# Kernel tuning notes

Measured on AMD Instinct MI355X. Metric: run time of the kernel, lower is better.

## Reference

```python
import jax, jax.numpy as jnp
import numpy as np

N = 2048      # nodes (= in_features = out_features, forced by h0 @ adj)
C = 512       # channels
B = 8         # batch
NNZ = 65536   # number of edges (avg degree 32)
NEG = -9e15   # masked-fill value from the source


def setup_inputs() -> dict:
    key = jax.random.key(0)
    k1, k2, k3, k4 = jax.random.split(key, 4)
    x = jax.random.normal(k1, (B, C, N), dtype=jnp.float32)
    # xavier_normal_ with gain=0.01: std = gain * sqrt(2/(fan_in+fan_out))
    std = 0.01 * float(np.sqrt(2.0 / (N + N)))
    W1 = jax.random.normal(k2, (N, N), dtype=jnp.float32) * std
    W2 = jax.random.normal(k3, (N, N), dtype=jnp.float32) * std
    # e is initialized to 1 in the source; perturb so softmax is non-trivial
    e = 1.0 + 0.1 * jax.random.normal(k4, (NNZ,), dtype=jnp.float32)
    # flat row-major indices of mask nonzeros, unique + sorted (matches adj[mask] = e)
    rng = np.random.default_rng(0)
    edge_idx = np.sort(rng.choice(N * N, size=NNZ, replace=False)).astype(np.int64)
    return {"x": x, "W1": W1, "W2": W2, "e": e, "edge_idx": jnp.asarray(edge_idx)}


def reference(x, W1, W2, e, edge_idx):
    # h0, h1: [B, C, N]
    h0 = jnp.matmul(x, W1)
    h1 = jnp.matmul(x, W2)
    # scatter per-edge logits into dense [N, N], masked positions = -9e15
    logits = jnp.full((N * N,), NEG, dtype=jnp.float32).at[edge_idx].set(e)
    A = jax.nn.softmax(logits.reshape(N, N), axis=1)  # row-wise softmax
    diag = jnp.diagonal(A)                 # A * I  (self term, diagonal scaling)
    A_off = A - jnp.diag(diag)             # A * (1 - I)  (neighbor term)
    # h0 @ (A*I) == h0 scaled per-node by diag; h1 @ (A*(1-I)) dense GEMM
    out = h0 * diag[None, None, :] + jnp.matmul(h1, A_off)
    return out  # [B, C, N]; torch squeeze is a no-op here; bias=False
```

## Files before the change

kernel.cpp:

```cpp
#include <hip/hip_runtime.h>
#include <hip/hip_bf16.h>
#include <stdint.h>

#define NN 2048
#define LOG2NN 11
#define GK 2048
#define GNC 2048

typedef __bf16 bf16x8 __attribute__((ext_vector_type(8)));
typedef float f32x4 __attribute__((ext_vector_type(4)));

__device__ __forceinline__ ushort f2bf(float f) {
  uint32_t x = __float_as_uint(f);
  uint32_t r = (x + 0x7fffu + ((x >> 16) & 1u)) >> 16;
  return (ushort)r;
}

__device__ __forceinline__ int lower_bound32(const int* __restrict__ a, int n, int v) {
  int lo = 0, hi = n;
  while (lo < hi) {
    int mid = (lo + hi) >> 1;
    if (a[mid] < v) lo = mid + 1; else hi = mid;
  }
  return lo;
}

__global__ __launch_bounds__(256) void prep_kernel(
    const float* __restrict__ W1, const float* __restrict__ W2,
    ushort* __restrict__ WT, ushort* __restrict__ W2T,
    int* __restrict__ hist, int* __restrict__ ecnt,
    const int* __restrict__ idx, const float* __restrict__ e, int nnz,
    float* __restrict__ vals, float* __restrict__ diag, int* __restrict__ empty) {
  __shared__ float tile[64][65];
  const int bid = blockIdx.x;
  const int t = threadIdx.x;
  if (bid < 2048) {
    const int m = bid >> 10;
    const int rem = bid & 1023;
    const int r0 = (rem >> 5) * 64, c0 = (rem & 31) * 64;
    const float* in = m ? W2 : W1;
    ushort* out = m ? W2T : WT;
    const int tx = t & 15, ty = t >> 4;
#pragma unroll
    for (int i = 0; i < 4; ++i) {
      int r = i * 16 + ty;
      float4 v = *reinterpret_cast<const float4*>(&in[(size_t)(r0 + r) * NN + c0 + tx * 4]);
      tile[r][tx * 4 + 0] = v.x;
      tile[r][tx * 4 + 1] = v.y;
      tile[r][tx * 4 + 2] = v.z;
      tile[r][tx * 4 + 3] = v.w;
    }
    __syncthreads();
#pragma unroll
    for (int i = 0; i < 4; ++i) {
      int oc = i * 16 + ty;
      ushort4 o;
      o.x = f2bf(tile[tx * 4 + 0][oc]);
      o.y = f2bf(tile[tx * 4 + 1][oc]);
      o.z = f2bf(tile[tx * 4 + 2][oc]);
      o.w = f2bf(tile[tx * 4 + 3][oc]);
      *reinterpret_cast<ushort4*>(&out[(size_t)(c0 + oc) * NN + r0 + tx * 4]) = o;
    }
  } else {
    const int w = t >> 6, lane = t & 63;
    const int r = (bid - 2048) * 4 + w;
    int lo = lower_bound32(idx, nnz, r << LOG2NN);
    int hi = lower_bound32(idx, nnz, (r + 1) << LOG2NN);
    if (hi <= lo) {
      if (lane == 0) { diag[r] = 1.0f / NN; empty[r] = 1; atomicAdd(ecnt, 1); }
      return;
    }
    float m = -3.0e38f;
    for (int j = lo + lane; j < hi; j += 64) m = fmaxf(m, e[j]);
#pragma unroll
    for (int s = 32; s >= 1; s >>= 1) m = fmaxf(m, __shfl_xor(m, s));
    float sum = 0.f;
    for (int j = lo + lane; j < hi; j += 64) sum += expf(e[j] - m);
#pragma unroll
    for (int s = 32; s >= 1; s >>= 1) sum += __shfl_xor(sum, s);
    float inv = 1.0f / sum;
    float dv = 0.f;
    for (int j = lo + lane; j < hi; j += 64) {
      float v = expf(e[j] - m) * inv;
      vals[j] = v;
      int c = idx[j] & (NN - 1);
      if (c == r) dv = v;
      else atomicAdd(&hist[c], 1);
    }
#pragma unroll
    for (int s = 32; s >= 1; s >>= 1) dv += __shfl_xor(dv, s);
    if (lane == 0) { diag[r] = dv; empty[r] = 0; }
  }
}

__global__ __launch_bounds__(256) void scan_uw_kernel(
    const int* __restrict__ hist, int* __restrict__ base, int* __restrict__ cursor,
    const float* __restrict__ W2, const int* __restrict__ empty,
    const int* __restrict__ ecnt, float* __restrict__ uW) {
  if (blockIdx.x == 0) {
    const int l = threadIdx.x;
    if (l >= 64) return;
    int vals[32], pre[32];
    int run = 0;
#pragma unroll
    for (int j = 0; j < 32; ++j) {
      vals[j] = hist[l * 32 + j];
      pre[j] = run;
      run += vals[j];
    }
    int tot = run, inc = run;
#pragma unroll
    for (int s = 1; s < 64; s <<= 1) {
      int o = __shfl_up(inc, s);
      if (l >= s) inc += o;
    }
    int excl = inc - tot;
#pragma unroll
    for (int j = 0; j < 32; ++j) {
      int b = excl + pre[j];
      base[l * 32 + j] = b;
      cursor[l * 32 + j] = b;
    }
  } else {
    if (*ecnt == 0) return;
    int p = (blockIdx.x - 1) * 256 + threadIdx.x;
    float s = 0.f;
    for (int k = 0; k < NN; ++k)
      if (empty[k]) s += W2[(size_t)p * NN + k];
    uW[p] = s * (1.0f / NN);
  }
}

__global__ void scatter_kernel(const int* __restrict__ idx, const float* __restrict__ vals,
                               int nnz, int* __restrict__ cursor,
                               int* __restrict__ ek, float* __restrict__ ev) {
  int j = blockIdx.x * blockDim.x + threadIdx.x;
  if (j >= nnz) return;
  int f = idx[j];
  int c = f & (NN - 1), r = f >> LOG2NN;
  if (c != r) {
    int p = atomicAdd(&cursor[c], 1);
    ek[p] = r;
    ev[p] = vals[j];
  }
}

__global__ __launch_bounds__(256) void spmm_kernel(
    const int* __restrict__ ek, const float* __restrict__ ev,
    const int* __restrict__ base, const int* __restrict__ hist,
    const ushort* __restrict__ W2T,
    const float* __restrict__ diag, const int* __restrict__ empty,
    const float* __restrict__ uW, ushort* WT,
    const float* __restrict__ x, ushort* __restrict__ xb) {
  if (blockIdx.x >= 1024) {
    int i = ((int)blockIdx.x - 1024) * 256 + threadIdx.x;
    const float4* in4 = reinterpret_cast<const float4*>(x);
    float4 a = in4[2 * i];
    float4 b = in4[2 * i + 1];
    uint4 o;
    o.x = (uint32_t)f2bf(a.x) | ((uint32_t)f2bf(a.y) << 16);
    o.y = (uint32_t)f2bf(a.z) | ((uint32_t)f2bf(a.w) << 16);
    o.z = (uint32_t)f2bf(b.x) | ((uint32_t)f2bf(b.y) << 16);
    o.w = (uint32_t)f2bf(b.z) | ((uint32_t)f2bf(b.w) << 16);
    reinterpret_cast<uint4*>(xb)[i] = o;
    return;
  }
  const int w = threadIdx.x >> 6, lane = threadIdx.x & 63;
  const int n = blockIdx.x * 2 + (w >> 1);
  const int c0 = (w & 1) * 1024 + lane * 16;
  const int start = base[n], cnt = hist[n];
  float acc[2][8];
#pragma unroll
  for (int g = 0; g < 2; ++g) {
    float4 u0 = *reinterpret_cast<const float4*>(&uW[c0 + g * 8]);
    float4 u1 = *reinterpret_cast<const float4*>(&uW[c0 + g * 8 + 4]);
    acc[g][0] = u0.x; acc[g][1] = u0.y; acc[g][2] = u0.z; acc[g][3] = u0.w;
    acc[g][4] = u1.x; acc[g][5] = u1.y; acc[g][6] = u1.z; acc[g][7] = u1.w;
  }
  float d = diag[n];
  if (d != 0.f) {
#pragma unroll
    for (int g = 0; g < 2; ++g) {
      bf16x8 wd = *reinterpret_cast<const bf16x8*>(&WT[(size_t)n * NN + c0 + g * 8]);
#pragma unroll
      for (int j = 0; j < 8; ++j) acc[g][j] += d * (float)wd[j];
    }
  }
  int i = 0;
  for (; i + 4 <= cnt; i += 4) {
    int k[4];
    float v[4];
    bf16x8 wv[4][2];
#pragma unroll
    for (int e2 = 0; e2 < 4; ++e2) {
      k[e2] = ek[start + i + e2];
      v[e2] = ev[start + i + e2];
    }
#pragma unroll
    for (int e2 = 0; e2 < 4; ++e2)
#pragma unroll
      for (int g = 0; g < 2; ++g)
        wv[e2][g] = *reinterpret_cast<const bf16x8*>(&W2T[(size_t)k[e2] * NN + c0 + g * 8]);
#pragma unroll
    for (int e2 = 0; e2 < 4; ++e2)
#pragma unroll
      for (int g = 0; g < 2; ++g)
#pragma unroll
        for (int j = 0; j < 8; ++j)
          acc[g][j] += v[e2] * (float)wv[e2][g][j];
  }
  for (; i < cnt; ++i) {
    int k0 = ek[start + i];
    float v0 = ev[start + i];
#pragma unroll
    for (int g = 0; g < 2; ++g) {
      bf16x8 w0 = *reinterpret_cast<const bf16x8*>(&W2T[(size_t)k0 * NN + c0 + g * 8]);
#pragma unroll
      for (int j = 0; j < 8; ++j) acc[g][j] += v0 * (float)w0[j];
    }
  }
  if (empty[n]) {
#pragma unroll
    for (int g = 0; g < 2; ++g) {
      bf16x8 we = *reinterpret_cast<const bf16x8*>(&W2T[(size_t)n * NN + c0 + g * 8]);
#pragma unroll
      for (int j = 0; j < 8; ++j) acc[g][j] -= (1.0f / NN) * (float)we[j];
    }
  }
#pragma unroll
  for (int g = 0; g < 2; ++g) {
    uint4 o;
    o.x = (uint32_t)f2bf(acc[g][0]) | ((uint32_t)f2bf(acc[g][1]) << 16);
    o.y = (uint32_t)f2bf(acc[g][2]) | ((uint32_t)f2bf(acc[g][3]) << 16);
    o.z = (uint32_t)f2bf(acc[g][4]) | ((uint32_t)f2bf(acc[g][5]) << 16);
    o.w = (uint32_t)f2bf(acc[g][6]) | ((uint32_t)f2bf(acc[g][7]) << 16);
    *reinterpret_cast<uint4*>(&WT[(size_t)n * NN + c0 + g * 8]) = o;
  }
}

__device__ __forceinline__ void gload_lds16(const ushort* g, char* l) {
  __builtin_amdgcn_global_load_lds(
      (__attribute__((address_space(1))) uint32_t*)(uintptr_t)g,
      (__attribute__((address_space(3))) uint32_t*)l, 16, 0, 0);
}

#define NT 32

__global__ __launch_bounds__(512, 2)
void gemm8_kernel(const ushort* __restrict__ A, const ushort* __restrict__ Bt,
                  float* __restrict__ Cf) {
  __shared__ __align__(16) char smem[98304];
  const int t = threadIdx.x;
  const int wid = t >> 6, lane = t & 63;
  const int wm = wid >> 1, wn = wid & 1;
  const int fr = lane & 15, fg = lane >> 4;

  const int swz = ((int)blockIdx.x & 7) * 32 + ((int)blockIdx.x >> 3);
  const int m0 = (swz >> 4) * 256;
  const int n0 = (swz & 15) * 128;

  const int l8 = lane >> 3;
  const int scol = ((lane & 7) ^ l8) << 3;
  const int srow = wid * 8 + l8;

#define STGA(H, TAU) do {                                                      \
    const int _b = (TAU) & 1;                                                  \
    gload_lds16(A + (size_t)(m0 + (H) * 128 + srow) * GK + (TAU) * 64 + scol,  \
                smem + _b * 32768 + (H) * 16384 + wid * 1024);                 \
    gload_lds16(A + (size_t)(m0 + (H) * 128 + 64 + srow) * GK + (TAU) * 64 + scol, \
                smem + _b * 32768 + (H) * 16384 + 8192 + wid * 1024);          \
  } while (0)

#define STGB(TAU) do {                                                         \
    const int _b = (TAU) & 1;                                                  \
    gload_lds16(Bt + (size_t)(n0 + srow) * GK + (TAU) * 64 + scol,             \
                smem + 65536 + _b * 16384 + wid * 1024);                       \
    gload_lds16(Bt + (size_t)(n0 + 64 + srow) * GK + (TAU) * 64 + scol,        \
                smem + 65536 + _b * 16384 + 8192 + wid * 1024);                \
  } while (0)

  const int sw = (fr & 7) << 4;
  const int ko0 = (fg * 16) ^ sw;
  const int ko1 = (64 + fg * 16) ^ sw;

  f32x4 acc[4][4] = {};

  STGA(0, 0); STGA(1, 0); STGB(0);
  STGA(0, 1); STGA(1, 1); STGB(1);
  asm volatile("s_waitcnt vmcnt(6)" ::: "memory");
  __builtin_amdgcn_s_barrier();
  asm volatile("" ::: "memory");

  for (int kt = 0; kt < NT; ++kt) {
    const int b = kt & 1;
    const int t2 = (kt + 2) & (NT - 1);
    const char* Ab = smem + b * 32768;
    const char* Bb = smem + 65536 + b * 16384;
    bf16x8 aF[4][2], bF[4][2];
#pragma unroll
    for (int mf = 0; mf < 4; ++mf) {
      const int row = wm * 64 + mf * 16 + fr;
      const char* p = Ab + (row >> 7) * 16384 + (row & 127) * 128;
      aF[mf][0] = *reinterpret_cast<const bf16x8*>(p + ko0);
    }
#pragma unroll
    for (int nf = 0; nf < 4; ++nf) {
      const char* p = Bb + (wn * 64 + nf * 16 + fr) * 128;
      bF[nf][0] = *reinterpret_cast<const bf16x8*>(p + ko0);
    }
#pragma unroll
    for (int mf = 0; mf < 4; ++mf) {
      const int row = wm * 64 + mf * 16 + fr;
      const char* p = Ab + (row >> 7) * 16384 + (row & 127) * 128;
      aF[mf][1] = *reinterpret_cast<const bf16x8*>(p + ko1);
    }
#pragma unroll
    for (int nf = 0; nf < 4; ++nf) {
      const char* p = Bb + (wn * 64 + nf * 16 + fr) * 128;
      bF[nf][1] = *reinterpret_cast<const bf16x8*>(p + ko1);
    }
    __builtin_amdgcn_s_setprio(1);
#pragma unroll
    for (int mf = 0; mf < 4; ++mf)
#pragma unroll
      for (int nf = 0; nf < 4; ++nf)
        acc[mf][nf] = __builtin_amdgcn_mfma_f32_16x16x32_bf16(
            aF[mf][0], bF[nf][0], acc[mf][nf], 0, 0, 0);
#pragma unroll
    for (int mf = 0; mf < 4; ++mf)
#pragma unroll
      for (int nf = 0; nf < 4; ++nf)
        acc[mf][nf] = __builtin_amdgcn_mfma_f32_16x16x32_bf16(
            aF[mf][1], bF[nf][1], acc[mf][nf], 0, 0, 0);
    __builtin_amdgcn_s_setprio(0);
    __builtin_amdgcn_s_barrier();
    asm volatile("" ::: "memory");
    STGA(0, t2); STGA(1, t2); STGB(t2);
    asm volatile("s_waitcnt vmcnt(6)" ::: "memory");
    __builtin_amdgcn_s_barrier();
    asm volatile("" ::: "memory");
  }

  asm volatile("s_waitcnt vmcnt(0)" ::: "memory");
  const int cr = lane >> 4, cc = lane & 15;
#pragma unroll
  for (int mf = 0; mf < 4; ++mf)
#pragma unroll
    for (int nf = 0; nf < 4; ++nf)
#pragma unroll
      for (int q = 0; q < 4; ++q) {
        int gm = m0 + wm * 64 + mf * 16 + cr * 4 + q;
        int gn = n0 + wn * 64 + nf * 16 + cc;
        Cf[(size_t)gm * GNC + gn] = acc[mf][nf][q];
      }
}

extern "C" void kernel_launch(void* const* d_in, const int* in_sizes, int n_in,
                              void* d_out, int out_size, void* d_ws, size_t ws_size,
                              hipStream_t stream) {
  const float* x   = (const float*)d_in[0];
  const float* W1  = (const float*)d_in[1];
  const float* W2  = (const float*)d_in[2];
  const float* e   = (const float*)d_in[3];
  const int*   eix = (const int*)d_in[4];
  const int nnz = in_sizes[3];
  float* out = (float*)d_out;

  char* w = (char*)d_ws;
  ushort* W2T  = (ushort*)w; w += (size_t)NN * NN * 2;
  ushort* WT   = (ushort*)w; w += (size_t)NN * NN * 2;
  ushort* xb   = (ushort*)w; w += (size_t)4096 * NN * 2;
  float*  vals = (float*)w;  w += (size_t)nnz * 4;
  int*    ek   = (int*)w;    w += (size_t)nnz * 4;
  float*  ev   = (float*)w;  w += (size_t)nnz * 4;
  int*    base = (int*)w;    w += NN * 4;
  int*    curs = (int*)w;    w += NN * 4;
  float*  diag = (float*)w;  w += NN * 4;
  int*    empt = (int*)w;    w += NN * 4;
  int*    hist = (int*)w;    w += NN * 4;
  float*  uW   = (float*)w;  w += NN * 4;
  int*    ecnt = (int*)w;    w += 256;

  hipMemsetAsync(hist, 0, NN * 4 + NN * 4 + 256, stream);

  prep_kernel<<<dim3(2560), dim3(256), 0, stream>>>(W1, W2, WT, W2T,
                                                    hist, ecnt,
                                                    eix, e, nnz, vals, diag, empt);
  scan_uw_kernel<<<dim3(9), dim3(256), 0, stream>>>(hist, base, curs, W2, empt,
                                                    ecnt, uW);
  scatter_kernel<<<dim3((nnz + 255) / 256), dim3(256), 0, stream>>>(eix, vals, nnz,
                                                                    curs, ek, ev);
  spmm_kernel<<<dim3(5120), dim3(256), 0, stream>>>(ek, ev, base, hist, W2T,
                                                    diag, empt, uW, WT, x, xb);
  gemm8_kernel<<<dim3(256), dim3(512), 0, stream>>>(xb, WT, out);
}
```

Measured before the change: 111.2 us.

## Split GEMM k-tile into two half-stages with finer-grained async prefetch

Reorganizes the shared-memory layout of the bf16 GEMM so each 64-wide k-tile is stored as two 32-wide halves, and issues global-to-LDS loads per half so they interleave with the MFMA work on the other half. The XOR swizzle is removed in favour of a plain 64-byte row stride, and fragment register usage is halved. The aim is to overlap memory transfer with compute more finely. In exchange it adds an extra barrier per half-step, and the unswizzled layout may cause LDS bank conflicts.

```diff
diff --git a/kernel.cpp b/kernel.cpp
--- a/kernel.cpp
+++ b/kernel.cpp
@@ -259,84 +259,83 @@
   const int m0 = (swz >> 4) * 256;
   const int n0 = (swz & 15) * 128;
 
-  const int l8 = lane >> 3;
-  const int scol = ((lane & 7) ^ l8) << 3;
-  const int srow = wid * 8 + l8;
-
-#define STGA(H, TAU) do {                                                      \
-    const int _b = (TAU) & 1;                                                  \
-    gload_lds16(A + (size_t)(m0 + (H) * 128 + srow) * GK + (TAU) * 64 + scol,  \
-                smem + _b * 32768 + (H) * 16384 + wid * 1024);                 \
-    gload_lds16(A + (size_t)(m0 + (H) * 128 + 64 + srow) * GK + (TAU) * 64 + scol, \
-                smem + _b * 32768 + (H) * 16384 + 8192 + wid * 1024);          \
-  } while (0)
-
-#define STGB(TAU) do {                                                         \
-    const int _b = (TAU) & 1;                                                  \
-    gload_lds16(Bt + (size_t)(n0 + srow) * GK + (TAU) * 64 + scol,             \
-                smem + 65536 + _b * 16384 + wid * 1024);                       \
-    gload_lds16(Bt + (size_t)(n0 + 64 + srow) * GK + (TAU) * 64 + scol,        \
-                smem + 65536 + _b * 16384 + 8192 + wid * 1024);                \
-  } while (0)
-
-  const int sw = (fr & 7) << 4;
-  const int ko0 = (fg * 16) ^ sw;
-  const int ko1 = (64 + fg * 16) ^ sw;
+  const int crow = wid * 16 + (lane >> 2);
+  const int ccol = (lane & 3) * 8;
+
+#define STGA(H, KS, TAU)                                                       \
+  gload_lds16(A + (size_t)(m0 + (H) * 128 + crow) * GK + (TAU) * 64 + (KS) * 32 + ccol, \
+              smem + ((TAU) & 1) * 32768 + (KS) * 16384 + (H) * 8192 + wid * 1024)
+#define STGB(KS, TAU)                                                          \
+  gload_lds16(Bt + (size_t)(n0 + crow) * GK + (TAU) * 64 + (KS) * 32 + ccol,   \
+              smem + 65536 + ((TAU) & 1) * 16384 + (KS) * 8192 + wid * 1024)
 
   f32x4 acc[4][4] = {};
 
-  STGA(0, 0); STGA(1, 0); STGB(0);
-  STGA(0, 1); STGA(1, 1); STGB(1);
+  STGA(0, 0, 0); STGA(1, 0, 0); STGB(0, 0);
+  STGA(0, 1, 0); STGA(1, 1, 0); STGB(1, 0);
+  STGA(0, 0, 1); STGA(1, 0, 1); STGB(0, 1);
   asm volatile("s_waitcnt vmcnt(6)" ::: "memory");
   __builtin_amdgcn_s_barrier();
   asm volatile("" ::: "memory");
 
   for (int kt = 0; kt < NT; ++kt) {
     const int b = kt & 1;
-    const int t2 = (kt + 2) & (NT - 1);
+    const int t1 = (kt + 1) & (NT - 1), t2 = (kt + 2) & (NT - 1);
     const char* Ab = smem + b * 32768;
     const char* Bb = smem + 65536 + b * 16384;
-    bf16x8 aF[4][2], bF[4][2];
+    bf16x8 aF[4], bF[4];
+
 #pragma unroll
     for (int mf = 0; mf < 4; ++mf) {
       const int row = wm * 64 + mf * 16 + fr;
-      const char* p = Ab + (row >> 7) * 16384 + (row & 127) * 128;
-      aF[mf][0] = *reinterpret_cast<const bf16x8*>(p + ko0);
+      aF[mf] = *reinterpret_cast<const bf16x8*>(
+          Ab + (row >> 7) * 8192 + (row & 127) * 64 + fg * 16);
     }
 #pragma unroll
     for (int nf = 0; nf < 4; ++nf) {
-      const char* p = Bb + (wn * 64 + nf * 16 + fr) * 128;
-      bF[nf][0] = *reinterpret_cast<const bf16x8*>(p + ko0);
-    }
-#pragma unroll
-    for (int mf = 0; mf < 4; ++mf) {
-      const int row = wm * 64 + mf * 16 + fr;
-      const char* p = Ab + (row >> 7) * 16384 + (row & 127) * 128;
-      aF[mf][1] = *reinterpret_cast<const bf16x8*>(p + ko1);
-    }
-#pragma unroll
-    for (int nf = 0; nf < 4; ++nf) {
-      const char* p = Bb + (wn * 64 + nf * 16 + fr) * 128;
-      bF[nf][1] = *reinterpret_cast<const bf16x8*>(p + ko1);
-    }
+      const int row = wn * 64 + nf * 16 + fr;
+      bF[nf] = *reinterpret_cast<const bf16x8*>(Bb + row * 64 + fg * 16);
+    }
+    STGA(0, 1, t1); STGA(1, 1, t1); STGB(1, t1);
+    asm volatile("s_waitcnt vmcnt(6)" ::: "memory");
+    __builtin_amdgcn_s_barrier();
+    asm volatile("s_waitcnt lgkmcnt(0)" ::: "memory");
+    __builtin_amdgcn_sched_barrier(0);
     __builtin_amdgcn_s_setprio(1);
 #pragma unroll
     for (int mf = 0; mf < 4; ++mf)
 #pragma unroll
       for (int nf = 0; nf < 4; ++nf)
         acc[mf][nf] = __builtin_amdgcn_mfma_f32_16x16x32_bf16(
-            aF[mf][0], bF[nf][0], acc[mf][nf], 0, 0, 0);
-#pragma unroll
-    for (int mf = 0; mf < 4; ++mf)
-#pragma unroll
-      for (int nf = 0; nf < 4; ++nf)
-        acc[mf][nf] = __builtin_amdgcn_mfma_f32_16x16x32_bf16(
-            aF[mf][1], bF[nf][1], acc[mf][nf], 0, 0, 0);
+            aF[mf], bF[nf], acc[mf][nf], 0, 0, 0);
     __builtin_amdgcn_s_setprio(0);
     __builtin_amdgcn_s_barrier();
     asm volatile("" ::: "memory");
-    STGA(0, t2); STGA(1, t2); STGB(t2);
+
+#pragma unroll
+    for (int mf = 0; mf < 4; ++mf) {
+      const int row = wm * 64 + mf * 16 + fr;
+      aF[mf] = *reinterpret_cast<const bf16x8*>(
+          Ab + 16384 + (row >> 7) * 8192 + (row & 127) * 64 + fg * 16);
+    }
+#pragma unroll
+    for (int nf = 0; nf < 4; ++nf) {
+      const int row = wn * 64 + nf * 16 + fr;
+      bF[nf] = *reinterpret_cast<const bf16x8*>(Bb + 8192 + row * 64 + fg * 16);
+    }
+    STGA(0, 0, t2); STGA(1, 0, t2); STGB(0, t2);
     asm volatile("s_waitcnt vmcnt(6)" ::: "memory");
+    __builtin_amdgcn_s_barrier();
+    asm volatile("s_waitcnt lgkmcnt(0)" ::: "memory");
+    __builtin_amdgcn_sched_barrier(0);
+    __builtin_amdgcn_s_setprio(1);
+#pragma unroll
+    for (int mf = 0; mf < 4; ++mf)
+#pragma unroll
+      for (int nf = 0; nf < 4; ++nf)
+        acc[mf][nf] = __builtin_amdgcn_mfma_f32_16x16x32_bf16(
+            aF[mf], bF[nf], acc[mf][nf], 0, 0, 0);
+    __builtin_amdgcn_s_setprio(0);
     __builtin_amdgcn_s_barrier();
     asm volatile("" ::: "memory");
   }
```

Result: slower. 113.6 us (+2.1%).

## Triple-buffer LDS in the bf16 GEMM and drop one barrier per k-step

Applied to the files above, without the earlier changes.

Grows the shared-memory staging area from two buffers to three (A and B tiles). Each iteration now issues the global-to-LDS copies for step k+2 before it reads the current tile, which removes the barrier that separated the MFMA loop from the prefetch. The aim is to overlap global loads with LDS reads and MFMA work, and to cut one workgroup synchronisation per iteration. The cost is 144KB of LDS per workgroup, which rules out a second resident workgroup per CU. The A and B fragment reads are also interleaved differently.

```diff
diff --git a/kernel.cpp b/kernel.cpp
--- a/kernel.cpp
+++ b/kernel.cpp
@@ -249,7 +249,7 @@
 __global__ __launch_bounds__(512, 2)
 void gemm8_kernel(const ushort* __restrict__ A, const ushort* __restrict__ Bt,
                   float* __restrict__ Cf) {
-  __shared__ __align__(16) char smem[98304];
+  __shared__ __align__(16) char smem[147456];
   const int t = threadIdx.x;
   const int wid = t >> 6, lane = t & 63;
   const int wm = wid >> 1, wn = wid & 1;
@@ -263,20 +263,18 @@
   const int scol = ((lane & 7) ^ l8) << 3;
   const int srow = wid * 8 + l8;
 
-#define STGA(H, TAU) do {                                                      \
-    const int _b = (TAU) & 1;                                                  \
+#define STGA(H, TAU, BUF) do {                                                 \
     gload_lds16(A + (size_t)(m0 + (H) * 128 + srow) * GK + (TAU) * 64 + scol,  \
-                smem + _b * 32768 + (H) * 16384 + wid * 1024);                 \
+                smem + (BUF) * 32768 + (H) * 16384 + wid * 1024);              \
     gload_lds16(A + (size_t)(m0 + (H) * 128 + 64 + srow) * GK + (TAU) * 64 + scol, \
-                smem + _b * 32768 + (H) * 16384 + 8192 + wid * 1024);          \
+                smem + (BUF) * 32768 + (H) * 16384 + 8192 + wid * 1024);       \
   } while (0)
 
-#define STGB(TAU) do {                                                         \
-    const int _b = (TAU) & 1;                                                  \
+#define STGB(TAU, BUF) do {                                                    \
     gload_lds16(Bt + (size_t)(n0 + srow) * GK + (TAU) * 64 + scol,             \
-                smem + 65536 + _b * 16384 + wid * 1024);                       \
+                smem + 98304 + (BUF) * 16384 + wid * 1024);                    \
     gload_lds16(Bt + (size_t)(n0 + 64 + srow) * GK + (TAU) * 64 + scol,        \
-                smem + 65536 + _b * 16384 + 8192 + wid * 1024);                \
+                smem + 98304 + (BUF) * 16384 + 8192 + wid * 1024);             \
   } while (0)
 
   const int sw = (fr & 7) << 4;
@@ -285,38 +283,32 @@
 
   f32x4 acc[4][4] = {};
 
-  STGA(0, 0); STGA(1, 0); STGB(0);
-  STGA(0, 1); STGA(1, 1); STGB(1);
+  STGA(0, 0, 0); STGA(1, 0, 0); STGB(0, 0);
+  STGA(0, 1, 1); STGA(1, 1, 1); STGB(1, 1);
   asm volatile("s_waitcnt vmcnt(6)" ::: "memory");
   __builtin_amdgcn_s_barrier();
   asm volatile("" ::: "memory");
 
   for (int kt = 0; kt < NT; ++kt) {
-    const int b = kt & 1;
+    const int br = kt % 3;
+    const int bs = (kt + 2) % 3;
     const int t2 = (kt + 2) & (NT - 1);
-    const char* Ab = smem + b * 32768;
-    const char* Bb = smem + 65536 + b * 16384;
+    STGA(0, t2, bs); STGA(1, t2, bs); STGB(t2, bs);
+
+    const char* Ab = smem + br * 32768;
+    const char* Bb = smem + 98304 + br * 16384;
     bf16x8 aF[4][2], bF[4][2];
 #pragma unroll
     for (int mf = 0; mf < 4; ++mf) {
       const int row = wm * 64 + mf * 16 + fr;
       const char* p = Ab + (row >> 7) * 16384 + (row & 127) * 128;
       aF[mf][0] = *reinterpret_cast<const bf16x8*>(p + ko0);
+      aF[mf][1] = *reinterpret_cast<const bf16x8*>(p + ko1);
     }
 #pragma unroll
     for (int nf = 0; nf < 4; ++nf) {
       const char* p = Bb + (wn * 64 + nf * 16 + fr) * 128;
       bF[nf][0] = *reinterpret_cast<const bf16x8*>(p + ko0);
-    }
-#pragma unroll
-    for (int mf = 0; mf < 4; ++mf) {
-      const int row = wm * 64 + mf * 16 + fr;
-      const char* p = Ab + (row >> 7) * 16384 + (row & 127) * 128;
-      aF[mf][1] = *reinterpret_cast<const bf16x8*>(p + ko1);
-    }
-#pragma unroll
-    for (int nf = 0; nf < 4; ++nf) {
-      const char* p = Bb + (wn * 64 + nf * 16 + fr) * 128;
       bF[nf][1] = *reinterpret_cast<const bf16x8*>(p + ko1);
     }
     __builtin_amdgcn_s_setprio(1);
@@ -333,9 +325,6 @@
         acc[mf][nf] = __builtin_amdgcn_mfma_f32_16x16x32_bf16(
             aF[mf][1], bF[nf][1], acc[mf][nf], 0, 0, 0);
     __builtin_amdgcn_s_setprio(0);
-    __builtin_amdgcn_s_barrier();
-    asm volatile("" ::: "memory");
-    STGA(0, t2); STGA(1, t2); STGB(t2);
     asm volatile("s_waitcnt vmcnt(6)" ::: "memory");
     __builtin_amdgcn_s_barrier();
     asm volatile("" ::: "memory");
```

New measurement: 106.5 us. 4.2% less time.
